# Performance work log

Hardware: AMD Instinct MI355X
Metric: run time of the kernel (lower is better)

Reference implementation:

```python
import jax, jax.numpy as jnp
import numpy as np

NUM_GROUPS = 32
EPS = 1e-5


def group_norm(x, w, b):
    # x: [B, C, H, W]
    B, C, H, W = x.shape
    xg = x.reshape(B, NUM_GROUPS, C // NUM_GROUPS, H, W)
    mean = jnp.mean(xg, axis=(2, 3, 4), keepdims=True)
    var = jnp.var(xg, axis=(2, 3, 4), keepdims=True)
    xg = (xg - mean) * jax.lax.rsqrt(var + EPS)
    xn = xg.reshape(B, C, H, W)
    return xn * w[None, :, None, None] + b[None, :, None, None]


def conv1x1(x, w, b):
    # x: [B, C, H, W], w: [O, C], b: [O]
    return jnp.einsum('bchw,oc->bohw', x, w) + b[None, :, None, None]


def setup_inputs() -> dict:
    key = jax.random.key(0)
    ks = jax.random.split(key, 10)
    C = 512
    x = jax.random.normal(ks[0], (4, C, 64, 64), dtype=jnp.float32)
    s = 1.0 / np.sqrt(C)
    return {
        'x': x,
        'gn_w': jnp.ones((C,), jnp.float32),
        'gn_b': jnp.zeros((C,), jnp.float32),
        'q_w': jax.random.normal(ks[1], (C, C), jnp.float32) * s,
        'q_b': jax.random.normal(ks[2], (C,), jnp.float32) * 0.01,
        'k_w': jax.random.normal(ks[3], (C, C), jnp.float32) * s,
        'k_b': jax.random.normal(ks[4], (C,), jnp.float32) * 0.01,
        'v_w': jax.random.normal(ks[5], (C, C), jnp.float32) * s,
        'v_b': jax.random.normal(ks[6], (C,), jnp.float32) * 0.01,
        'p_w': jax.random.normal(ks[7], (C, C), jnp.float32) * s,
        'p_b': jax.random.normal(ks[8], (C,), jnp.float32) * 0.01,
    }


def reference(x, gn_w, gn_b, q_w, q_b, k_w, k_b, v_w, v_b, p_w, p_b):
    h_ = group_norm(x, gn_w, gn_b)
    q = conv1x1(h_, q_w, q_b)
    k = conv1x1(h_, k_w, k_b)
    v = conv1x1(h_, v_w, v_b)
    b, c, h, w = q.shape
    n = h * w
    q = q.reshape(b, c, n).transpose(0, 2, 1)   # [b, n, c]
    k = k.reshape(b, c, n)                       # [b, c, n]
    scores = jnp.einsum('bic,bcj->bij', q, k) * (c ** -0.5)  # [b, n, n]
    attn = jax.nn.softmax(scores, axis=-1)
    v = v.reshape(b, c, n)                       # [b, c, n]
    # h_[b,c,i] = sum_j v[b,c,j] * attn[b,i,j]
    h_out = jnp.einsum('bcj,bij->bci', v, attn).reshape(b, c, h, w)
    return x + conv1x1(h_out, p_w, p_b)
```

## Files before the change

### kernel.cpp

```cpp
#include <hip/hip_runtime.h>
#include <hip/hip_bf16.h>
#include <stdint.h>

#define AS1 __attribute__((address_space(1)))
#define AS3 __attribute__((address_space(3)))

typedef unsigned short ushort_t;
typedef __attribute__((ext_vector_type(8))) short short8;
typedef __attribute__((ext_vector_type(4))) float floatx4;
typedef __attribute__((ext_vector_type(16))) float floatx16;
typedef __attribute__((ext_vector_type(2))) unsigned int uint2v;

__device__ __forceinline__ ushort_t f2b(float f) {
    union { float f; unsigned int i; } x; x.f = f;
    unsigned int r = x.i + 0x7fffu + ((x.i >> 16) & 1u);
    return (ushort_t)(r >> 16);
}
__device__ __forceinline__ float b2f(ushort_t u) {
    union { unsigned int i; float f; } x; x.i = ((unsigned int)u) << 16; return x.f;
}
__device__ __forceinline__ void gl2lds16(const void* g, void* l) {
    __builtin_amdgcn_global_load_lds(
        (const AS1 unsigned int*)g,
        (AS3 unsigned int*)l,
        16, 0, 0);
}
__device__ __forceinline__ void plswap(unsigned& a, unsigned& b) {
#if __has_builtin(__builtin_amdgcn_permlane32_swap)
    uint2v r = __builtin_amdgcn_permlane32_swap(a, b, false, false);
    a = r.x; b = r.y;
#else
    asm volatile("v_permlane32_swap_b32 %0, %1" : "+v"(a), "+v"(b));
#endif
}

static constexpr int CCH = 512;
static constexpr int NSP = 4096;
static constexpr int NG  = 32;

__global__ __launch_bounds__(256) void gn_stats(const float* __restrict__ x,
                                                float* __restrict__ mean,
                                                float* __restrict__ rstd) {
    const long base = (long)blockIdx.x * 65536;
    const int t = threadIdx.x;
    float s1 = 0.f, s2 = 0.f;
    for (int i = t * 8; i < 65536; i += 256 * 8) {
        float4 a = *(const float4*)(x + base + i);
        float4 b = *(const float4*)(x + base + i + 4);
        s1 += a.x + a.y + a.z + a.w + b.x + b.y + b.z + b.w;
        s2 += a.x * a.x + a.y * a.y + a.z * a.z + a.w * a.w
            + b.x * b.x + b.y * b.y + b.z * b.z + b.w * b.w;
    }
#pragma unroll
    for (int o = 32; o; o >>= 1) { s1 += __shfl_xor(s1, o, 64); s2 += __shfl_xor(s2, o, 64); }
    __shared__ float r1[4], r2[4];
    const int lane = t & 63, wave = t >> 6;
    if (!lane) { r1[wave] = s1; r2[wave] = s2; }
    __syncthreads();
    if (!t) {
        float S1 = r1[0] + r1[1] + r1[2] + r1[3];
        float S2 = r2[0] + r2[1] + r2[2] + r2[3];
        float mu = S1 * (1.f / 65536.f);
        float var = S2 * (1.f / 65536.f) - mu * mu;
        mean[blockIdx.x] = mu;
        rstd[blockIdx.x] = rsqrtf(var + 1e-5f);
    }
}

__global__ __launch_bounds__(256) void w_to_bf16(const float* __restrict__ q,
                                                 const float* __restrict__ k,
                                                 const float* __restrict__ v,
                                                 const float* __restrict__ p,
                                                 const float* __restrict__ qb,
                                                 ushort_t* __restrict__ out,
                                                 float* __restrict__ sqb) {
    const float scl = 0.044194173824159216f;
    const float* srcs[4] = { q, k, v, p };
    const float* s = srcs[blockIdx.y];
    const float m = (blockIdx.y == 0) ? scl : 1.f;
    const long i = ((long)blockIdx.x * 256 + threadIdx.x) * 4;
    float4 f = *(const float4*)(s + i);
    ushort_t o[4] __attribute__((aligned(8)));
    o[0] = f2b(f.x * m); o[1] = f2b(f.y * m); o[2] = f2b(f.z * m); o[3] = f2b(f.w * m);
    *(ushort4*)(out + (long)blockIdx.y * 262144 + i) = *(ushort4*)o;
    if (blockIdx.y == 0 && blockIdx.x == 0 && threadIdx.x < 128) {
        const int j = threadIdx.x * 4;
        float4 b = *(const float4*)(qb + j);
        sqb[j] = b.x * scl; sqb[j + 1] = b.y * scl; sqb[j + 2] = b.z * scl; sqb[j + 3] = b.w * scl;
    }
}

__global__ __launch_bounds__(256) void norm_transpose(const float* __restrict__ x,
                                                      const float* __restrict__ gw,
                                                      const float* __restrict__ gb,
                                                      const float* __restrict__ mean,
                                                      const float* __restrict__ rstd,
                                                      ushort_t* __restrict__ ht) {
    __shared__ ushort_t tile[64 * 65];
    const int b = blockIdx.z, c0 = blockIdx.y * 64, n0 = blockIdx.x * 64;
    const int t = threadIdx.x;
    const float* xb = x + ((long)b * CCH + c0) * NSP + n0;
#pragma unroll
    for (int p = 0; p < 2; ++p) {
        int li = p * 2048 + t * 8;
        int cl = li >> 6, nl = li & 63;
        int c = c0 + cl, g = c >> 4;
        float mu = mean[b * NG + g], rs = rstd[b * NG + g];
        float w  = gw[c] * rs;
        float bb = gb[c] - mu * w;
        float4 a = *(const float4*)(xb + (long)cl * NSP + nl);
        float4 d = *(const float4*)(xb + (long)cl * NSP + nl + 4);
        float f[8] = { a.x, a.y, a.z, a.w, d.x, d.y, d.z, d.w };
#pragma unroll
        for (int j = 0; j < 8; ++j) tile[cl * 65 + nl + j] = f2b(f[j] * w + bb);
    }
    __syncthreads();
#pragma unroll
    for (int p = 0; p < 2; ++p) {
        int li = p * 2048 + t * 8;
        int nl = li >> 6, cl = li & 63;
        ushort_t v[8] __attribute__((aligned(16)));
#pragma unroll
        for (int j = 0; j < 8; ++j) v[j] = tile[(cl + j) * 65 + nl];
        *(uint4*)(ht + ((long)b * NSP + n0 + nl) * CCH + c0 + cl) = *(uint4*)v;
    }
}

template <int BIAS, int OUTF32, int RES>
__global__ __launch_bounds__(256, 2) void gemm_tn(
    const ushort_t* __restrict__ A, int lda, long sA,
    const ushort_t* __restrict__ B, int ldb, long sB,
    void* __restrict__ Cp, int ldc, long sC,
    const float* __restrict__ bias,
    const float* __restrict__ resid, long sR,
    float scale, int K) {
    __shared__ short As[128 * 32];
    __shared__ short Bs[128 * 32];
    const int t = threadIdx.x;
    const int lane = t & 63, wave = t >> 6;
    const long bz = blockIdx.z;
    const int m0 = blockIdx.y * 128, n0 = blockIdx.x * 128;

    const ushort_t* Ab = A + bz * sA + (long)(m0 + (t >> 2)) * lda + (t & 3) * 8;
    const ushort_t* Bb = B + bz * sB + (long)(n0 + (t >> 2)) * ldb + (t & 3) * 8;
    short* la = As + t * 8;
    short* lb = Bs + t * 8;

    const int wm = (wave & 1) * 64, wn = (wave >> 1) * 64;
    const int lm = lane & 15, lk = (lane >> 4) * 8;
    const short* pa = As + (wm + lm) * 32 + lk;
    const short* pb = Bs + (wn + lm) * 32 + lk;

    floatx4 acc[4][4];
#pragma unroll
    for (int i = 0; i < 4; ++i)
#pragma unroll
        for (int j = 0; j < 4; ++j) acc[i][j] = (floatx4){0.f, 0.f, 0.f, 0.f};

    for (int k0 = 0; k0 < K; k0 += 32) {
        __syncthreads();
        gl2lds16(Ab, la);
        gl2lds16(Ab + 64 * (long)lda, la + 64 * 32);
        gl2lds16(Bb, lb);
        gl2lds16(Bb + 64 * (long)ldb, lb + 64 * 32);
        Ab += 32; Bb += 32;
        __builtin_amdgcn_s_waitcnt(0);
        __syncthreads();
        short8 af[4], bfr[4];
#pragma unroll
        for (int i = 0; i < 4; ++i) af[i]  = *(const short8*)(pa + i * 16 * 32);
#pragma unroll
        for (int i = 0; i < 4; ++i) bfr[i] = *(const short8*)(pb + i * 16 * 32);
#pragma unroll
        for (int mi = 0; mi < 4; ++mi)
#pragma unroll
            for (int ni = 0; ni < 4; ++ni)
                acc[mi][ni] = __builtin_amdgcn_mfma_f32_16x16x32_bf16(af[mi], bfr[ni], acc[mi][ni], 0, 0, 0);
    }

    const int row4 = (lane >> 4) * 4;
    const int ncol = lane & 15;
#pragma unroll
    for (int mi = 0; mi < 4; ++mi) {
#pragma unroll
        for (int ni = 0; ni < 4; ++ni) {
            const int n = n0 + wn + ni * 16 + ncol;
            float bn = (BIAS == 2) ? bias[n] : 0.f;
#pragma unroll
            for (int r = 0; r < 4; ++r) {
                const int m = m0 + wm + mi * 16 + row4 + r;
                float v = acc[mi][ni][r] * scale;
                if (BIAS == 1) v += bias[m];
                if (BIAS == 2) v += bn;
                if (RES) v += resid[bz * sR + (long)m * ldc + n];
                const long idx = bz * sC + (long)m * ldc + n;
                if (OUTF32) ((float*)Cp)[idx] = v;
                else        ((ushort_t*)Cp)[idx] = f2b(v);
            }
        }
    }
}

__global__ __launch_bounds__(256, 1) void flash_attn(const ushort_t* __restrict__ Qt,
                                                     const ushort_t* __restrict__ Kt,
                                                     const ushort_t* __restrict__ V,
                                                     ushort_t* __restrict__ pO0,
                                                     ushort_t* __restrict__ pO1,
                                                     float* __restrict__ ml) {
    __shared__ short Klds[2 * 16384];
    __shared__ short Vlds[2 * 16384];
    const int t = threadIdx.x;
    const int lane = t & 63, wave = t >> 6;
    const int l31 = lane & 31, hi = lane >> 5;
    const int blk = blockIdx.x;
    const int xcd = blk & 7;
    const int bb = xcd >> 1;
    const int split = xcd & 1;
    const int rows0 = (blk >> 3) * 128 + wave * 32;
    const int j_lo = split * 2048;

    const ushort_t* Qb = Qt + ((long)bb * NSP + rows0 + l31) * CCH + hi * 8;
    short8 qf[32];
#pragma unroll
    for (int s = 0; s < 32; ++s) qf[s] = *(const short8*)(Qb + s * 16);

    floatx16 acc[16];
#pragma unroll
    for (int i = 0; i < 16; ++i)
        acc[i] = (floatx16){0.f,0.f,0.f,0.f,0.f,0.f,0.f,0.f,0.f,0.f,0.f,0.f,0.f,0.f,0.f,0.f};
    float lsum = 0.f;

    const ushort_t* KtB = Kt + (long)bb * NSP * CCH;
    const ushort_t* Vb  = V + (long)bb * NSP * CCH;

#define STAGE_K(buf, J0)                                                          \
    {                                                                             \
        short* kb_ = Klds + (buf) * 16384;                                        \
        _Pragma("unroll")                                                         \
        for (int i_ = 0; i_ < 8; ++i_) {                                          \
            const int ch_ = i_ * 256 + t;                                         \
            const int jr_ = ch_ >> 6, m_ = ch_ & 63;                              \
            const int ms_ = m_ ^ ((jr_ & 7) << 1);                                \
            gl2lds16(KtB + (long)((J0) + jr_) * CCH + ms_ * 8, kb_ + ch_ * 8);    \
        }                                                                         \
    }
#define STAGE_V(buf, J0)                                                          \
    {                                                                             \
        short* vb_ = Vlds + (buf) * 16384;                                        \
        _Pragma("unroll")                                                         \
        for (int i_ = 0; i_ < 8; ++i_) {                                          \
            const int g_ = i_ * 256 + t;                                          \
            const int d_ = g_ >> 2, mv_ = g_ & 3;                                 \
            const int js_ = (mv_ ^ ((d_ >> 1) & 3)) * 8;                          \
            gl2lds16(Vb + (long)d_ * NSP + (J0) + js_, vb_ + g_ * 8);             \
        }                                                                         \
    }

    STAGE_K(0, j_lo);
    STAGE_V(0, j_lo);
    __builtin_amdgcn_s_waitcnt(0);
    __syncthreads();

    const int jj = l31 & 7;
    const int cv = (l31 >> 1) & 3;
    const int koff = l31 * 512 + hi * 8;
    const int voff0 = l31 * 32 + ((hi ^ cv) << 3);
    const int voff1 = l31 * 32 + (((2 + hi) ^ cv) << 3);

    int j0 = j_lo;
    for (int tile = 0; tile < 64; ++tile) {
        const int cur = tile & 1;
        if (tile + 1 < 64) {
            STAGE_K(cur ^ 1, j0 + 32);
            STAGE_V(cur ^ 1, j0 + 32);
        }
        const short* kp = Klds + cur * 16384 + koff;

        floatx16 sE = (floatx16){0.f,0.f,0.f,0.f,0.f,0.f,0.f,0.f,0.f,0.f,0.f,0.f,0.f,0.f,0.f,0.f};
        floatx16 sO = sE;
#pragma unroll
        for (int s2 = 0; s2 < 16; ++s2) {
            short8 k0 = *(const short8*)(kp + (((2 * s2)     ^ jj) << 4));
            short8 k1 = *(const short8*)(kp + (((2 * s2 + 1) ^ jj) << 4));
            sE = __builtin_amdgcn_mfma_f32_32x32x16_bf16(k0, qf[2 * s2],     sE, 0, 0, 0);
            sO = __builtin_amdgcn_mfma_f32_32x32x16_bf16(k1, qf[2 * s2 + 1], sO, 0, 0, 0);
        }

        float pv_[16];
#pragma unroll
        for (int r = 0; r < 16; ++r) { pv_[r] = __expf(sE[r] + sO[r] - 12.f); lsum += pv_[r]; }
        unsigned pk[8];
#pragma unroll
        for (int g = 0; g < 4; ++g) {
            asm("v_cvt_pk_bf16_f32 %0, %1, %2" : "=v"(pk[2 * g])     : "v"(pv_[4 * g]),     "v"(pv_[4 * g + 1]));
            asm("v_cvt_pk_bf16_f32 %0, %1, %2" : "=v"(pk[2 * g + 1]) : "v"(pv_[4 * g + 2]), "v"(pv_[4 * g + 3]));
        }
        plswap(pk[0], pk[2]);
        plswap(pk[1], pk[3]);
        plswap(pk[4], pk[6]);
        plswap(pk[5], pk[7]);
        union { unsigned u[4]; short8 s8; } uA, uB;
        uA.u[0] = pk[0]; uA.u[1] = pk[1]; uA.u[2] = pk[2]; uA.u[3] = pk[3];
        uB.u[0] = pk[4]; uB.u[1] = pk[5]; uB.u[2] = pk[6]; uB.u[3] = pk[7];
        const short8 PA0 = uA.s8;
        const short8 PA1 = uB.s8;

        const short* vp0 = Vlds + cur * 16384 + voff0;
        const short* vp1 = Vlds + cur * 16384 + voff1;
#pragma unroll
        for (int dt = 0; dt < 16; ++dt) {
            short8 v0 = *(const short8*)(vp0 + dt * 1024);
            acc[dt] = __builtin_amdgcn_mfma_f32_32x32x16_bf16(PA0, v0, acc[dt], 0, 0, 0);
        }
#pragma unroll
        for (int dt = 0; dt < 16; ++dt) {
            short8 v1 = *(const short8*)(vp1 + dt * 1024);
            acc[dt] = __builtin_amdgcn_mfma_f32_32x32x16_bf16(PA1, v1, acc[dt], 0, 0, 0);
        }
        __builtin_amdgcn_s_waitcnt(0);
        __syncthreads();
        j0 += 32;
    }
#undef STAGE_K
#undef STAGE_V

    const float lt = lsum + __shfl_xor(lsum, 32, 64);
    ushort_t* pOut = (split ? pO1 : pO0) + ((long)bb * NSP + rows0) * CCH;
#pragma unroll
    for (int dt = 0; dt < 16; ++dt)
#pragma unroll
        for (int r = 0; r < 16; ++r) {
            const int rl = (r & 3) + 8 * (r >> 2) + 4 * hi;
            pOut[(long)rl * CCH + dt * 32 + l31] = f2b(acc[dt][r]);
        }
    if (hi == 0) {
        ml[(long)split * 4 * NSP + (long)bb * NSP + rows0 + l31] = lt;
    }
}

__global__ __launch_bounds__(256) void merge_splits(ushort_t* __restrict__ pO0,
                                                    const ushort_t* __restrict__ pO1,
                                                    const float* __restrict__ ml) {
    const long f = ((long)blockIdx.x * 256 + threadIdx.x) * 8;
    const long row = f >> 9;
    const float inv = 1.f / (ml[row] + ml[(long)4 * NSP + row]);
    uint4 u0 = *(const uint4*)(pO0 + f);
    uint4 u1 = *(const uint4*)(pO1 + f);
    const unsigned int* a = (const unsigned int*)&u0;
    const unsigned int* b = (const unsigned int*)&u1;
    ushort_t out[8] __attribute__((aligned(16)));
#pragma unroll
    for (int i = 0; i < 4; ++i) {
        float x0 = __uint_as_float(a[i] << 16), y0 = __uint_as_float(a[i] & 0xffff0000u);
        float x1 = __uint_as_float(b[i] << 16), y1 = __uint_as_float(b[i] & 0xffff0000u);
        out[2 * i]     = f2b((x0 + x1) * inv);
        out[2 * i + 1] = f2b((y0 + y1) * inv);
    }
    *(uint4*)(pO0 + f) = *(uint4*)out;
}

extern "C" void kernel_launch(void* const* d_in, const int* in_sizes, int n_in,
                              void* d_out, int out_size, void* d_ws, size_t ws_size,
                              hipStream_t stream) {
    const float* x   = (const float*)d_in[0];
    const float* gnw = (const float*)d_in[1];
    const float* gnb = (const float*)d_in[2];
    const float* qw  = (const float*)d_in[3];
    const float* qb  = (const float*)d_in[4];
    const float* kw  = (const float*)d_in[5];
    const float* kb  = (const float*)d_in[6];
    const float* vw  = (const float*)d_in[7];
    const float* vb  = (const float*)d_in[8];
    const float* pw  = (const float*)d_in[9];
    const float* pb  = (const float*)d_in[10];
    float* out = (float*)d_out;
    (void)in_sizes; (void)n_in; (void)out_size; (void)ws_size;

    const long E = (long)NSP * CCH;
    char* ws = (char*)d_ws;
    float*    mean = (float*)ws;
    float*    rstd = (float*)(ws + 512);
    ushort_t* wb   = (ushort_t*)(ws + 1024);
    float*    sqb  = (float*)(wb + 4 * 262144);
    float*    ml   = sqb + 512;
    ushort_t* ht   = (ushort_t*)(ml + 2 * 4 * NSP);
    ushort_t* Kt   = ht + 4 * E;
    ushort_t* V    = Kt + 4 * E;
    ushort_t* Qt   = V  + 4 * E;
    ushort_t* hOT  = Qt + 4 * E;
    ushort_t* qwb = wb, *kwb = wb + 262144, *vwb = wb + 2 * 262144, *pwb = wb + 3 * 262144;

    gn_stats<<<128, 256, 0, stream>>>(x, mean, rstd);
    w_to_bf16<<<dim3(256, 4), 256, 0, stream>>>(qw, kw, vw, pw, qb, wb, sqb);
    norm_transpose<<<dim3(64, 8, 4), 256, 0, stream>>>(x, gnw, gnb, mean, rstd, ht);
    gemm_tn<2, 0, 0><<<dim3(4, 32, 4), 256, 0, stream>>>(ht, 512, E, qwb, 512, 0, Qt, 512, E, sqb, nullptr, 0, 1.f, 512);
    gemm_tn<2, 0, 0><<<dim3(4, 32, 4), 256, 0, stream>>>(ht, 512, E, kwb, 512, 0, Kt, 512, E, kb, nullptr, 0, 1.f, 512);
    gemm_tn<1, 0, 0><<<dim3(32, 4, 4), 256, 0, stream>>>(vwb, 512, 0, ht, 512, E, V, 4096, E, vb, nullptr, 0, 1.f, 512);
    flash_attn<<<256, 256, 0, stream>>>(Qt, Kt, V, hOT, ht, ml);
    merge_splits<<<4096, 256, 0, stream>>>(hOT, ht, ml);
    gemm_tn<1, 1, 1><<<dim3(32, 4, 4), 256, 0, stream>>>(pwb, 512, 0, hOT, 512, E,
                                                         out, 4096, E, pb, x, E, 1.f, 512);
}
```

Baseline: 390.5 us.

## Load V fragments directly from global memory instead of staging through LDS

The flash attention kernel no longer stages V tiles into a double-buffered LDS region. Each lane reads its V MFMA operands straight from global memory into registers, and the second half is prefetched while the first-half MFMAs run. The K LDS swizzle is changed to a 16-way XOR pattern, and the two partial score accumulators are summed before the exponential. This frees half the LDS and removes the V LDS traffic, but it adds global-load latency inside the loop, uses more registers, and relies on cache hits for V that all four waves share.

```diff
diff --git a/kernel.cpp b/kernel.cpp
--- a/kernel.cpp
+++ b/kernel.cpp
@@ -208,7 +208,6 @@
                                                      ushort_t* __restrict__ pO1,
                                                      float* __restrict__ ml) {
     __shared__ short Klds[2 * 16384];
-    __shared__ short Vlds[2 * 16384];
     const int t = threadIdx.x;
     const int lane = t & 63, wave = t >> 6;
     const int l31 = lane & 31, hi = lane >> 5;
@@ -231,7 +230,7 @@
     float lsum = 0.f;
 
     const ushort_t* KtB = Kt + (long)bb * NSP * CCH;
-    const ushort_t* Vb  = V + (long)bb * NSP * CCH;
+    const ushort_t* vgt = V + (long)bb * NSP * CCH + (long)l31 * NSP + hi * 8 + j_lo;
 
 #define STAGE_K(buf, J0)                                                          \
     {                                                                             \
@@ -240,55 +239,45 @@
         for (int i_ = 0; i_ < 8; ++i_) {                                          \
             const int ch_ = i_ * 256 + t;                                         \
             const int jr_ = ch_ >> 6, m_ = ch_ & 63;                              \
-            const int ms_ = m_ ^ ((jr_ & 7) << 1);                                \
+            const int ms_ = m_ ^ (jr_ & 15);                                      \
             gl2lds16(KtB + (long)((J0) + jr_) * CCH + ms_ * 8, kb_ + ch_ * 8);    \
         }                                                                         \
     }
-#define STAGE_V(buf, J0)                                                          \
-    {                                                                             \
-        short* vb_ = Vlds + (buf) * 16384;                                        \
-        _Pragma("unroll")                                                         \
-        for (int i_ = 0; i_ < 8; ++i_) {                                          \
-            const int g_ = i_ * 256 + t;                                          \
-            const int d_ = g_ >> 2, mv_ = g_ & 3;                                 \
-            const int js_ = (mv_ ^ ((d_ >> 1) & 3)) * 8;                          \
-            gl2lds16(Vb + (long)d_ * NSP + (J0) + js_, vb_ + g_ * 8);             \
-        }                                                                         \
-    }
 
     STAGE_K(0, j_lo);
-    STAGE_V(0, j_lo);
     __builtin_amdgcn_s_waitcnt(0);
     __syncthreads();
 
-    const int jj = l31 & 7;
-    const int cv = (l31 >> 1) & 3;
-    const int koff = l31 * 512 + hi * 8;
-    const int voff0 = l31 * 32 + ((hi ^ cv) << 3);
-    const int voff1 = l31 * 32 + (((2 + hi) ^ cv) << 3);
+    const int exr = (l31 & 15) ^ hi;
+    const short* kroot = Klds + l31 * 512;
 
     int j0 = j_lo;
     for (int tile = 0; tile < 64; ++tile) {
         const int cur = tile & 1;
         if (tile + 1 < 64) {
             STAGE_K(cur ^ 1, j0 + 32);
-            STAGE_V(cur ^ 1, j0 + 32);
-        }
-        const short* kp = Klds + cur * 16384 + koff;
+        }
+        const short* kp = kroot + cur * 16384;
 
         floatx16 sE = (floatx16){0.f,0.f,0.f,0.f,0.f,0.f,0.f,0.f,0.f,0.f,0.f,0.f,0.f,0.f,0.f,0.f};
         floatx16 sO = sE;
 #pragma unroll
         for (int s2 = 0; s2 < 16; ++s2) {
-            short8 k0 = *(const short8*)(kp + (((2 * s2)     ^ jj) << 4));
-            short8 k1 = *(const short8*)(kp + (((2 * s2 + 1) ^ jj) << 4));
+            short8 k0 = *(const short8*)(kp + (((4 * s2)     ^ exr) << 3));
+            short8 k1 = *(const short8*)(kp + (((4 * s2 + 2) ^ exr) << 3));
             sE = __builtin_amdgcn_mfma_f32_32x32x16_bf16(k0, qf[2 * s2],     sE, 0, 0, 0);
             sO = __builtin_amdgcn_mfma_f32_32x32x16_bf16(k1, qf[2 * s2 + 1], sO, 0, 0, 0);
         }
+        sE += sO;
+
+        short8 vr[16];
+#pragma unroll
+        for (int dt = 0; dt < 16; ++dt)
+            vr[dt] = *(const short8*)(vgt + (long)dt * (32 * NSP));
 
         float pv_[16];
 #pragma unroll
-        for (int r = 0; r < 16; ++r) { pv_[r] = __expf(sE[r] + sO[r] - 12.f); lsum += pv_[r]; }
+        for (int r = 0; r < 16; ++r) { pv_[r] = __expf(sE[r] - 12.f); lsum += pv_[r]; }
         unsigned pk[8];
 #pragma unroll
         for (int g = 0; g < 4; ++g) {
@@ -305,24 +294,21 @@
         const short8 PA0 = uA.s8;
         const short8 PA1 = uB.s8;
 
-        const short* vp0 = Vlds + cur * 16384 + voff0;
-        const short* vp1 = Vlds + cur * 16384 + voff1;
 #pragma unroll
         for (int dt = 0; dt < 16; ++dt) {
-            short8 v0 = *(const short8*)(vp0 + dt * 1024);
-            acc[dt] = __builtin_amdgcn_mfma_f32_32x32x16_bf16(PA0, v0, acc[dt], 0, 0, 0);
+            acc[dt] = __builtin_amdgcn_mfma_f32_32x32x16_bf16(PA0, vr[dt], acc[dt], 0, 0, 0);
+            vr[dt] = *(const short8*)(vgt + (long)dt * (32 * NSP) + 16);
         }
 #pragma unroll
         for (int dt = 0; dt < 16; ++dt) {
-            short8 v1 = *(const short8*)(vp1 + dt * 1024);
-            acc[dt] = __builtin_amdgcn_mfma_f32_32x32x16_bf16(PA1, v1, acc[dt], 0, 0, 0);
+            acc[dt] = __builtin_amdgcn_mfma_f32_32x32x16_bf16(PA1, vr[dt], acc[dt], 0, 0, 0);
         }
         __builtin_amdgcn_s_waitcnt(0);
         __syncthreads();
         j0 += 32;
+        vgt += 32;
     }
 #undef STAGE_K
-#undef STAGE_V
 
     const float lt = lsum + __shfl_xor(lsum, 32, 64);
     ushort_t* pOut = (split ? pO1 : pO0) + ((long)bb * NSP + rows0) * CCH;
```

Result: slower. 585.5 us (+49.9%).
